# Kernel optimization log

Measured on AMD Instinct MI355X. Metric: run time of the kernel, lower is better.

Reference implementation:

```python
import jax, jax.numpy as jnp
import numpy as np

B, L, C = 256, 196, 768      # batch, tokens (14x14 grid), token_dim
K = 2048                      # codebook size (num_tokens)
H = W = 14                    # h = int(sqrt(L)), w = L // h


def setup_inputs() -> dict:
    key = jax.random.key(0)
    k1, k2, k3 = jax.random.split(key, 3)
    in_feas = jax.random.normal(k1, (B, L, C), dtype=jnp.float32)
    codebook = jax.random.normal(k2, (K, C), dtype=jnp.float32)
    # Conv1d(in=C, out=1, kernel=3, padding=1, bias=False) weight: [1, C, 3]
    att_w = jax.random.normal(k3, (1, C, 3), dtype=jnp.float32) * 0.02
    return {"in_feas": in_feas, "codebook": codebook, "att_w": att_w}


def reference(in_feas, codebook, att_w):
    b, l, c = in_feas.shape
    flat = in_feas.reshape(-1, c)  # [B*L, C]

    # --- SOHO visual-dictionary (VQ) nearest-neighbour lookup ---
    d = (jnp.sum(flat * flat, axis=1, keepdims=True)
         - 2.0 * flat @ codebook.T
         + jnp.sum(codebook * codebook, axis=1)[None, :])  # [B*L, K]
    encoding_indices = jnp.argmin(d, axis=1)               # [B*L] int
    quantized = codebook[encoding_indices]                 # [B*L, C]
    # straight-through estimator: output = x + sg(q - x)
    vd_outputs = flat + jax.lax.stop_gradient(quantized - flat)

    idx_out = encoding_indices.reshape(-1, H, W)

    # --- attention branch (att=True, not_plus=False) ---
    # Conv1d(C->1, k=3, pad=1) applied to each token as a length-1 sequence:
    # only the center tap att_w[0, :, 1] multiplies real data (neighbors are
    # zero padding), so the conv reduces to a dot with the center weights.
    att = jax.nn.relu(vd_outputs @ att_w[0, :, 1])         # [B*L]
    att_mask = jax.nn.softmax(att.reshape(b, l, 1), axis=1)  # softmax over L

    vd_outputs = vd_outputs.reshape(b, l, c)
    out_feas = vd_outputs + in_feas * att_mask
    return out_feas, idx_out
```

## Files before the change

### kernel.cpp

```cpp
#include <hip/hip_runtime.h>

#define B_ 256
#define L_ 196
#define C_ 768
#define K_ 2048
#define BL_ 50176

typedef __attribute__((ext_vector_type(8))) short bf16x8;
typedef __attribute__((ext_vector_type(4))) float f32x4;

typedef const __attribute__((address_space(1))) void gas_void;
typedef __attribute__((address_space(3))) void las_void;

__device__ __forceinline__ unsigned short f2bf(float f) {
  unsigned u = __builtin_bit_cast(unsigned, f);
  u = u + 0x7FFFu + ((u >> 16) & 1u);
  return (unsigned short)(u >> 16);
}

__device__ __forceinline__ unsigned fmono(float f) {
  unsigned u = __builtin_bit_cast(unsigned, f);
  return u ^ ((unsigned)((int)u >> 31) | 0x80000000u);
}

__global__ __launch_bounds__(256) void precompute_kernel(
    const float* __restrict__ cb, const float* __restrict__ attw,
    unsigned short* __restrict__ cbb, double* __restrict__ norms64,
    float* __restrict__ norms32, float* __restrict__ ac) {
  int wave = threadIdx.x >> 6;
  int lane = threadIdx.x & 63;
  int k = blockIdx.x * 4 + wave;
  const float* row = cb + (size_t)k * C_;
  double n = 0.0, a = 0.0;
  for (int c = lane; c < C_; c += 64) {
    float v = row[c];
    cbb[(size_t)k * C_ + c] = f2bf(v);
    n = fma((double)v, (double)v, n);
    a = fma((double)v, (double)attw[c * 3 + 1], a);
  }
  for (int off = 32; off > 0; off >>= 1) {
    n += __shfl_down(n, off);
    a += __shfl_down(a, off);
  }
  if (lane == 0) {
    norms64[k] = n;
    norms32[k] = (float)n;
    ac[k] = (a > 0.0) ? (float)a : 0.0f;
  }
}

__global__ __launch_bounds__(256) void convert_kernel(
    const float* __restrict__ x, unsigned short* __restrict__ xb) {
  int i = blockIdx.x * 256 + threadIdx.x;
  float4 v = ((const float4*)x)[i];
  uint2 w;
  w.x = (unsigned)f2bf(v.x) | ((unsigned)f2bf(v.y) << 16);
  w.y = (unsigned)f2bf(v.z) | ((unsigned)f2bf(v.w) << 16);
  ((uint2*)xb)[i] = w;
}

__global__ __launch_bounds__(512, 2) void phase1_kernel(
    const unsigned short* __restrict__ xb,
    const unsigned short* __restrict__ cbb,
    const float* __restrict__ norms32, unsigned* __restrict__ ws_cand) {
  __shared__ unsigned short lds[2][2][2][128 * 64];
  __shared__ float norms_s[256];
  __shared__ unsigned cands_s[256][12];

  int tid = threadIdx.x;
  int bid = blockIdx.x;
  int x8 = bid & 7, m = bid >> 3;
  int mblk, nblk;
  if (m < 192) {
    mblk = (m & ~7) | x8;
    nblk = m & 7;
  } else {
    mblk = m;
    nblk = x8;
  }
  size_t row0 = (size_t)mblk * 256;
  int code0 = nblk * 256;

  int wv = tid >> 6, l = tid & 63;
  int wm = wv >> 2, wn = wv & 3;
  int col16 = l & 15, quad = l >> 4;

  if (tid < 256) norms_s[tid] = norms32[code0 + tid];

  int slotraw = (tid & 7) ^ ((tid >> 3) & 7);
  const unsigned short* abase = xb + (row0 + (tid >> 3)) * (size_t)C_ +
                                (size_t)slotraw * 8;
  const unsigned short* bbase = cbb + ((size_t)code0 + (tid >> 3)) * C_ +
                                (size_t)slotraw * 8;

  auto stageA = [&](int kt, int half, int buf) {
    const unsigned short* s =
        abase + (size_t)half * 128 * C_ + (size_t)kt * 64;
    char* d = (char*)&lds[buf][0][half][0] + wv * 1024;
    __builtin_amdgcn_global_load_lds((gas_void*)s, (las_void*)d, 16, 0, 0);
    __builtin_amdgcn_global_load_lds((gas_void*)(s + (size_t)64 * C_),
                                     (las_void*)(d + 8192), 16, 0, 0);
  };
  auto stageB = [&](int kt, int half, int buf) {
    const unsigned short* s =
        bbase + (size_t)half * 128 * C_ + (size_t)kt * 64;
    char* d = (char*)&lds[buf][1][half][0] + wv * 1024;
    __builtin_amdgcn_global_load_lds((gas_void*)s, (las_void*)d, 16, 0, 0);
    __builtin_amdgcn_global_load_lds((gas_void*)(s + (size_t)64 * C_),
                                     (las_void*)(d + 8192), 16, 0, 0);
  };

  f32x4 acc[2][2][4][2];
#pragma unroll
  for (int mh = 0; mh < 2; ++mh)
#pragma unroll
    for (int nh = 0; nh < 2; ++nh)
#pragma unroll
      for (int mt = 0; mt < 4; ++mt)
#pragma unroll
        for (int nt = 0; nt < 2; ++nt)
          acc[mh][nh][mt][nt] = (f32x4){0.f, 0.f, 0.f, 0.f};

  bf16x8 af[4][2], bfr[2][2];

#define LOADA(P)                                                            \
  _Pragma("unroll") for (int mt = 0; mt < 4; ++mt)                          \
      _Pragma("unroll") for (int ks = 0; ks < 2; ++ks) af[mt][ks] =         \
      *(const bf16x8*)((P) + (wm * 64 + mt * 16 + col16) * 128 +            \
                       (((ks * 4 + quad) ^ (col16 & 7)) * 16));

#define LOADB(P)                                                            \
  _Pragma("unroll") for (int nt = 0; nt < 2; ++nt)                          \
      _Pragma("unroll") for (int ks = 0; ks < 2; ++ks) bfr[nt][ks] =        \
      *(const bf16x8*)((P) + (wn * 32 + nt * 16 + col16) * 128 +            \
                       (((ks * 4 + quad) ^ (col16 & 7)) * 16));

#define MFMA_Q(mh, nh)                                                      \
  __builtin_amdgcn_s_setprio(1);                                            \
  _Pragma("unroll") for (int mt = 0; mt < 4; ++mt)                          \
      _Pragma("unroll") for (int nt = 0; nt < 2; ++nt)                      \
          _Pragma("unroll") for (int ks = 0; ks < 2; ++ks) acc[mh][nh][mt]  \
      [nt] = __builtin_amdgcn_mfma_f32_16x16x32_bf16(                       \
          af[mt][ks], bfr[nt][ks], acc[mh][nh][mt][nt], 0, 0, 0);           \
  __builtin_amdgcn_s_setprio(0);

  stageA(0, 0, 0);
  stageB(0, 0, 0);
  stageB(0, 1, 0);
  stageA(0, 1, 0);
  asm volatile("s_waitcnt vmcnt(4)" ::: "memory");
  __builtin_amdgcn_s_barrier();

  for (int t = 0; t < 12; ++t) {
    int buf = t & 1;
    const char* A0p = (const char*)&lds[buf][0][0][0];
    const char* A1p = (const char*)&lds[buf][0][1][0];
    const char* B0p = (const char*)&lds[buf][1][0][0];
    const char* B1p = (const char*)&lds[buf][1][1][0];
    bool st = (t < 11);

    if (st) {
      stageA(t + 1, 0, buf ^ 1);
      stageB(t + 1, 0, buf ^ 1);
    }
    LOADA(A0p);
    LOADB(B0p);
    MFMA_Q(0, 0);
    if (st) {
      asm volatile("s_waitcnt vmcnt(6)" ::: "memory");
    } else {
      asm volatile("s_waitcnt vmcnt(2)" ::: "memory");
    }
    __builtin_amdgcn_s_barrier();

    if (st) stageB(t + 1, 1, buf ^ 1);
    LOADB(B1p);
    MFMA_Q(0, 1);
    if (st) {
      asm volatile("s_waitcnt vmcnt(6)" ::: "memory");
    } else {
      asm volatile("s_waitcnt vmcnt(0)" ::: "memory");
    }
    __builtin_amdgcn_s_barrier();

    if (st) stageA(t + 1, 1, buf ^ 1);
    LOADA(A1p);
    MFMA_Q(1, 1);
    LOADB(B0p);
    MFMA_Q(1, 0);
    if (st) {
      asm volatile("s_waitcnt vmcnt(4)" ::: "memory");
    }
    __builtin_amdgcn_s_barrier();
  }

#undef LOADA
#undef LOADB
#undef MFMA_Q

#pragma unroll
  for (int mh = 0; mh < 2; ++mh) {
#pragma unroll
    for (int mt = 0; mt < 4; ++mt) {
#pragma unroll
      for (int r = 0; r < 4; ++r) {
        unsigned keys[4];
#pragma unroll
        for (int nh = 0; nh < 2; ++nh)
#pragma unroll
          for (int nt = 0; nt < 2; ++nt) {
            int codel = nh * 128 + wn * 32 + nt * 16 + col16;
            float d = fmaf(-2.0f, acc[mh][nh][mt][nt][r], norms_s[codel]);
            keys[nh * 2 + nt] =
                (fmono(d) & 0xFFFFF800u) | (unsigned)(code0 + codel);
          }
        unsigned win[3];
#pragma unroll
        for (int rnd = 0; rnd < 3; ++rnd) {
          unsigned mn = min(min(keys[0], keys[1]), min(keys[2], keys[3]));
          mn = min(mn, (unsigned)__shfl_xor((int)mn, 1));
          mn = min(mn, (unsigned)__shfl_xor((int)mn, 2));
          mn = min(mn, (unsigned)__shfl_xor((int)mn, 4));
          mn = min(mn, (unsigned)__shfl_xor((int)mn, 8));
          win[rnd] = mn;
#pragma unroll
          for (int nt = 0; nt < 4; ++nt)
            if (keys[nt] == mn) keys[nt] = 0xFFFFFFFFu;
        }
        if (col16 == 0) {
          int t = mh * 128 + wm * 64 + mt * 16 + quad * 4 + r;
          cands_s[t][wn * 3 + 0] = win[0];
          cands_s[t][wn * 3 + 1] = win[1];
          cands_s[t][wn * 3 + 2] = win[2];
        }
      }
    }
  }
  __syncthreads();
  for (int i = tid; i < 256 * 12; i += 512) {
    int t = i / 12;
    int j = i - t * 12;
    ws_cand[(row0 + t) * 96 + nblk * 12 + j] = cands_s[t][j];
  }
}

__global__ __launch_bounds__(256) void phase2_kernel(
    const float* __restrict__ x, const float* __restrict__ cb,
    const unsigned* __restrict__ ws_cand, const double* __restrict__ norms64,
    int* __restrict__ out_idx) {
  __shared__ unsigned cl[32][100];
  __shared__ int rcode[32][6];
  __shared__ double rd[32][6];
  int tid = threadIdx.x;
  size_t tok0 = (size_t)blockIdx.x * 32;

  for (int i = tid; i < 32 * 96; i += 256) {
    int t = i / 96;
    int s = i - t * 96;
    cl[t][s] = ws_cand[tok0 * 96 + i];
  }
  __syncthreads();

  if (tid < 32) {
    unsigned best[6];
#pragma unroll
    for (int j = 0; j < 6; ++j) best[j] = 0xFFFFFFFFu;
    for (int s = 0; s < 96; ++s) {
      unsigned v = cl[tid][s];
      if (v < best[5]) {
        best[5] = v;
#pragma unroll
        for (int j = 5; j > 0; --j) {
          if (best[j] < best[j - 1]) {
            unsigned t = best[j];
            best[j] = best[j - 1];
            best[j - 1] = t;
          }
        }
      }
    }
#pragma unroll
    for (int j = 0; j < 6; ++j) rcode[tid][j] = (int)(best[j] & 0x7FFu);
  }
  __syncthreads();

  if (tid < 192) {
    int t = tid / 6;
    int j = tid - t * 6;
    int code = rcode[t][j];
    const float* xr = x + (tok0 + t) * (size_t)C_;
    const float* cr = cb + (size_t)code * C_;
    double s = 0.0;
    for (int c = 0; c < C_; c += 4) {
      float4 xa = *(const float4*)(xr + c);
      float4 ca = *(const float4*)(cr + c);
      s = fma((double)xa.x, (double)ca.x, s);
      s = fma((double)xa.y, (double)ca.y, s);
      s = fma((double)xa.z, (double)ca.z, s);
      s = fma((double)xa.w, (double)ca.w, s);
    }
    rd[t][j] = fma(-2.0, s, norms64[code]);
  }
  __syncthreads();

  if (tid < 32) {
    double bv = rd[tid][0];
    int bi = rcode[tid][0];
#pragma unroll
    for (int j = 1; j < 6; ++j) {
      double v = rd[tid][j];
      int i0 = rcode[tid][j];
      if (v < bv || (v == bv && i0 < bi)) {
        bv = v;
        bi = i0;
      }
    }
    out_idx[tok0 + tid] = bi;
  }
}

#define APAD 776
__global__ __launch_bounds__(256, 2) void argmin_fallback(
    const float* __restrict__ x, const float* __restrict__ cb,
    const unsigned short* __restrict__ cbb,
    const double* __restrict__ norms64, const float* __restrict__ norms32,
    int* __restrict__ out_idx) {
  __shared__ unsigned short Asf[32 * APAD];
  __shared__ float norms_s[K_];
  __shared__ unsigned int cands[32][48];
  __shared__ int rcode[32][6];
  __shared__ double rd[32][6];

  int tid = threadIdx.x;
  size_t tok0 = (size_t)blockIdx.x * 32;

  for (int i = tid; i < K_; i += 256) norms_s[i] = norms32[i];

  const float4* xin = (const float4*)(x + tok0 * C_);
  for (int i = tid; i < 32 * 192; i += 256) {
    int tok = i / 192;
    int c4 = i - tok * 192;
    float4 v = xin[i];
    uint2 w;
    w.x = (unsigned)f2bf(v.x) | ((unsigned)f2bf(v.y) << 16);
    w.y = (unsigned)f2bf(v.z) | ((unsigned)f2bf(v.w) << 16);
    *(uint2*)&Asf[tok * APAD + c4 * 4] = w;
  }
  __syncthreads();

  int wv = tid >> 6;
  int lane = tid & 63;
  int col = lane & 15;
  int quad = lane >> 4;

  const unsigned short* a0p = &Asf[(col)*APAD + quad * 8];
  const unsigned short* a1p = &Asf[(16 + col) * APAD + quad * 8];

  for (int chunk = 0; chunk < 4; ++chunk) {
    int code0 = chunk * 512 + wv * 128 + col;
    const unsigned short* bbase = cbb + (size_t)code0 * C_ + quad * 8;

    f32x4 acc[2][8];
#pragma unroll
    for (int m = 0; m < 2; ++m)
#pragma unroll
      for (int n = 0; n < 8; ++n) acc[m][n] = (f32x4){0.f, 0.f, 0.f, 0.f};

    bf16x8 ca0 = *(const bf16x8*)(a0p);
    bf16x8 ca1 = *(const bf16x8*)(a1p);
    bf16x8 cbf[8];
#pragma unroll
    for (int n = 0; n < 8; ++n)
      cbf[n] = *(const bf16x8*)(bbase + (size_t)n * 16 * C_);

    for (int ks = 0; ks < 24; ++ks) {
      bf16x8 na0, na1, nbf[8];
      if (ks < 23) {
        int k1 = (ks + 1) * 32;
        na0 = *(const bf16x8*)(a0p + k1);
        na1 = *(const bf16x8*)(a1p + k1);
#pragma unroll
        for (int n = 0; n < 8; ++n)
          nbf[n] = *(const bf16x8*)(bbase + (size_t)n * 16 * C_ + k1);
      }
#pragma unroll
      for (int n = 0; n < 8; ++n) {
        acc[0][n] = __builtin_amdgcn_mfma_f32_16x16x32_bf16(ca0, cbf[n],
                                                            acc[0][n], 0, 0, 0);
        acc[1][n] = __builtin_amdgcn_mfma_f32_16x16x32_bf16(ca1, cbf[n],
                                                            acc[1][n], 0, 0, 0);
      }
      if (ks < 23) {
        ca0 = na0;
        ca1 = na1;
#pragma unroll
        for (int n = 0; n < 8; ++n) cbf[n] = nbf[n];
      }
    }

#pragma unroll
    for (int m = 0; m < 2; ++m) {
#pragma unroll
      for (int r = 0; r < 4; ++r) {
        unsigned keys[8];
#pragma unroll
        for (int n = 0; n < 8; ++n) {
          int code = code0 + n * 16;
          float d = fmaf(-2.0f, acc[m][n][r], norms_s[code]);
          keys[n] = (fmono(d) & 0xFFFFF800u) | (unsigned)code;
        }
        unsigned win[3];
#pragma unroll
        for (int rnd = 0; rnd < 3; ++rnd) {
          unsigned mn = keys[0];
#pragma unroll
          for (int n = 1; n < 8; ++n) mn = min(mn, keys[n]);
          mn = min(mn, (unsigned)__shfl_xor((int)mn, 1));
          mn = min(mn, (unsigned)__shfl_xor((int)mn, 2));
          mn = min(mn, (unsigned)__shfl_xor((int)mn, 4));
          mn = min(mn, (unsigned)__shfl_xor((int)mn, 8));
          win[rnd] = mn;
#pragma unroll
          for (int n = 0; n < 8; ++n)
            if (keys[n] == mn) keys[n] = 0xFFFFFFFFu;
        }
        if (col == 0) {
          int token = m * 16 + quad * 4 + r;
          unsigned* cp = &cands[token][chunk * 12 + wv * 3];
          cp[0] = win[0];
          cp[1] = win[1];
          cp[2] = win[2];
        }
      }
    }
  }
  __syncthreads();

  if (tid < 32) {
    unsigned best[6];
#pragma unroll
    for (int j = 0; j < 6; ++j) best[j] = 0xFFFFFFFFu;
    for (int s = 0; s < 48; ++s) {
      unsigned v = cands[tid][s];
      if (v < best[5]) {
        best[5] = v;
#pragma unroll
        for (int j = 5; j > 0; --j) {
          if (best[j] < best[j - 1]) {
            unsigned t = best[j];
            best[j] = best[j - 1];
            best[j - 1] = t;
          }
        }
      }
    }
#pragma unroll
    for (int j = 0; j < 6; ++j) rcode[tid][j] = (int)(best[j] & 0x7FFu);
  }
  __syncthreads();

  if (tid < 192) {
    int t = tid / 6;
    int j = tid - t * 6;
    int code = rcode[t][j];
    const float* xr = x + (tok0 + t) * (size_t)C_;
    const float* cr = cb + (size_t)code * C_;
    double s = 0.0;
    for (int c = 0; c < C_; c += 4) {
      float4 xa = *(const float4*)(xr + c);
      float4 ca = *(const float4*)(cr + c);
      s = fma((double)xa.x, (double)ca.x, s);
      s = fma((double)xa.y, (double)ca.y, s);
      s = fma((double)xa.z, (double)ca.z, s);
      s = fma((double)xa.w, (double)ca.w, s);
    }
    rd[t][j] = fma(-2.0, s, norms64[code]);
  }
  __syncthreads();

  if (tid < 32) {
    double bv = rd[tid][0];
    int bi = rcode[tid][0];
#pragma unroll
    for (int j = 1; j < 6; ++j) {
      double v = rd[tid][j];
      int i0 = rcode[tid][j];
      if (v < bv || (v == bv && i0 < bi)) {
        bv = v;
        bi = i0;
      }
    }
    out_idx[tok0 + tid] = bi;
  }
}

__global__ __launch_bounds__(1024) void epilogue_kernel(
    const float* __restrict__ x, const float* __restrict__ cb,
    const float* __restrict__ ac, const int* __restrict__ idx,
    float* __restrict__ out, float* __restrict__ out_idx) {
  __shared__ float att[256];
  __shared__ float red[256];
  __shared__ int ids[L_];
  int b = blockIdx.x;
  int tid = threadIdx.x;

  float e = 0.0f;
  if (tid < 256) {
    float a = -1e30f;
    if (tid < L_) {
      int myid = idx[b * L_ + tid];
      ids[tid] = myid;
      a = ac[myid];
    }
    att[tid] = a;
    red[tid] = a;
  }
  __syncthreads();
  for (int s = 128; s > 0; s >>= 1) {
    if (tid < s) red[tid] = fmaxf(red[tid], red[tid + s]);
    __syncthreads();
  }
  float mx = red[0];
  __syncthreads();
  if (tid < 256) {
    e = (tid < L_) ? expf(att[tid] - mx) : 0.0f;
    red[tid] = e;
  }
  __syncthreads();
  for (int s = 128; s > 0; s >>= 1) {
    if (tid < s) red[tid] += red[tid + s];
    __syncthreads();
  }
  float sum = red[0];
  __syncthreads();
  if (tid < 256) att[tid] = e / sum;
  __syncthreads();

  const float4* xin = (const float4*)(x + (size_t)b * L_ * C_);
  float4* o = (float4*)(out + (size_t)b * L_ * C_);
  for (int i = tid; i < L_ * (C_ / 4); i += 1024) {
    int l = i / (C_ / 4);
    int c4 = i - l * (C_ / 4);
    const float4* crow = (const float4*)(cb + (size_t)ids[l] * C_);
    float4 xv = xin[i];
    float4 cv = crow[c4];
    float mk = att[l];
    float4 ov;
    ov.x = cv.x + xv.x * mk;
    ov.y = cv.y + xv.y * mk;
    ov.z = cv.z + xv.z * mk;
    ov.w = cv.w + xv.w * mk;
    o[i] = ov;
  }
  if (tid < L_) out_idx[b * L_ + tid] = (float)ids[tid];
}

extern "C" void kernel_launch(void* const* d_in, const int* in_sizes, int n_in,
                              void* d_out, int out_size, void* d_ws,
                              size_t ws_size, hipStream_t stream) {
  const float* in_feas = (const float*)d_in[0];
  const float* cb = (const float*)d_in[1];
  const float* attw = (const float*)d_in[2];

  char* ws = (char*)d_ws;
  size_t off = 0;
  unsigned short* cbb = (unsigned short*)(ws + off); off += 3145728;
  double* norms64 = (double*)(ws + off);           off += 16384;
  float* norms32 = (float*)(ws + off);             off += 8192;
  float* ac = (float*)(ws + off);                  off += 8192;
  int* idx = (int*)(ws + off);                     off += 200704;
  size_t base = off;
  unsigned short* xb = (unsigned short*)(ws + off); off += (size_t)BL_ * C_ * 2;
  unsigned* ws_cand = (unsigned*)(ws + off);        off += (size_t)BL_ * 96 * 4;
  size_t need_full = off;

  float* out = (float*)d_out;
  float* out_idx = out + (size_t)B_ * L_ * C_;

  precompute_kernel<<<K_ / 4, 256, 0, stream>>>(cb, attw, cbb, norms64,
                                                norms32, ac);
  if (ws_size >= need_full) {
    convert_kernel<<<BL_ * C_ / 4 / 256, 256, 0, stream>>>(in_feas, xb);
    phase1_kernel<<<dim3((BL_ / 256) * (K_ / 256)), 512, 0, stream>>>(
        xb, cbb, norms32, ws_cand);
    phase2_kernel<<<BL_ / 32, 256, 0, stream>>>(in_feas, cb, ws_cand, norms64,
                                                idx);
  } else {
    argmin_fallback<<<BL_ / 32, 256, 0, stream>>>(in_feas, cb, cbb, norms64,
                                                  norms32, idx);
  }
  epilogue_kernel<<<B_, 1024, 0, stream>>>(in_feas, cb, ac, idx, out, out_idx);
  (void)base;
}
```

Baseline: 777.9 us.

## Register-staged GEMM pipeline and split phase2 rescoring dot products across lanes

The phase1 GEMM stops using direct global-to-LDS loads with fine-grained vmcnt waits. It now loads the next K tile into registers, writes it to the other LDS buffer in the middle and at the end of the MFMA sequence, and uses a single __syncthreads per iteration. MFMA fragments are now loaded per k-slice, which uses fewer registers, and the setprio hints are dropped. Phase2 runs 768 threads and gives each candidate dot product to 4 lanes with shuffle reductions, raising parallelism in the double-precision rescoring. The trade-offs are extra register pressure for staging and more LDS write traffic in the GEMM.

```diff
diff --git a/kernel.cpp b/kernel.cpp
--- a/kernel.cpp
+++ b/kernel.cpp
@@ -93,21 +93,38 @@
   const unsigned short* bbase = cbb + ((size_t)code0 + (tid >> 3)) * C_ +
                                 (size_t)slotraw * 8;
 
-  auto stageA = [&](int kt, int half, int buf) {
-    const unsigned short* s =
-        abase + (size_t)half * 128 * C_ + (size_t)kt * 64;
-    char* d = (char*)&lds[buf][0][half][0] + wv * 1024;
-    __builtin_amdgcn_global_load_lds((gas_void*)s, (las_void*)d, 16, 0, 0);
-    __builtin_amdgcn_global_load_lds((gas_void*)(s + (size_t)64 * C_),
-                                     (las_void*)(d + 8192), 16, 0, 0);
+  uint4 aA[2][2], bB[2][2];
+  auto issueA = [&](int kt) {
+#pragma unroll
+    for (int h = 0; h < 2; ++h)
+#pragma unroll
+      for (int i = 0; i < 2; ++i)
+        aA[h][i] = *(const uint4*)(abase + (size_t)h * 128 * C_ +
+                                   (size_t)i * 64 * C_ + kt * 64);
   };
-  auto stageB = [&](int kt, int half, int buf) {
-    const unsigned short* s =
-        bbase + (size_t)half * 128 * C_ + (size_t)kt * 64;
-    char* d = (char*)&lds[buf][1][half][0] + wv * 1024;
-    __builtin_amdgcn_global_load_lds((gas_void*)s, (las_void*)d, 16, 0, 0);
-    __builtin_amdgcn_global_load_lds((gas_void*)(s + (size_t)64 * C_),
-                                     (las_void*)(d + 8192), 16, 0, 0);
+  auto issueB = [&](int kt) {
+#pragma unroll
+    for (int h = 0; h < 2; ++h)
+#pragma unroll
+      for (int i = 0; i < 2; ++i)
+        bB[h][i] = *(const uint4*)(bbase + (size_t)h * 128 * C_ +
+                                   (size_t)i * 64 * C_ + kt * 64);
+  };
+  auto writeA = [&](int wb) {
+#pragma unroll
+    for (int h = 0; h < 2; ++h)
+#pragma unroll
+      for (int i = 0; i < 2; ++i)
+        *(uint4*)((char*)&lds[wb][0][h][0] + i * 8192 + (size_t)tid * 16) =
+            aA[h][i];
+  };
+  auto writeB = [&](int wb) {
+#pragma unroll
+    for (int h = 0; h < 2; ++h)
+#pragma unroll
+      for (int i = 0; i < 2; ++i)
+        *(uint4*)((char*)&lds[wb][1][h][0] + i * 8192 + (size_t)tid * 16) =
+            bB[h][i];
   };
 
   f32x4 acc[2][2][4][2];
@@ -121,82 +138,67 @@
         for (int nt = 0; nt < 2; ++nt)
           acc[mh][nh][mt][nt] = (f32x4){0.f, 0.f, 0.f, 0.f};
 
-  bf16x8 af[4][2], bfr[2][2];
-
-#define LOADA(P)                                                            \
-  _Pragma("unroll") for (int mt = 0; mt < 4; ++mt)                          \
-      _Pragma("unroll") for (int ks = 0; ks < 2; ++ks) af[mt][ks] =         \
-      *(const bf16x8*)((P) + (wm * 64 + mt * 16 + col16) * 128 +            \
-                       (((ks * 4 + quad) ^ (col16 & 7)) * 16));
-
-#define LOADB(P)                                                            \
-  _Pragma("unroll") for (int nt = 0; nt < 2; ++nt)                          \
-      _Pragma("unroll") for (int ks = 0; ks < 2; ++ks) bfr[nt][ks] =        \
-      *(const bf16x8*)((P) + (wn * 32 + nt * 16 + col16) * 128 +            \
-                       (((ks * 4 + quad) ^ (col16 & 7)) * 16));
-
-#define MFMA_Q(mh, nh)                                                      \
-  __builtin_amdgcn_s_setprio(1);                                            \
+  bf16x8 af[4], bfr[2];
+
+#define LOADA(mh, ks)                                                       \
+  _Pragma("unroll") for (int mt = 0; mt < 4; ++mt) af[mt] =                 \
+      *(const bf16x8*)((const char*)&lds[buf][0][mh][0] +                   \
+                       (wm * 64 + mt * 16 + col16) * 128 +                  \
+                       ((((ks)*4 + quad) ^ (col16 & 7)) * 16));
+
+#define LOADB(nh, ks)                                                       \
+  _Pragma("unroll") for (int nt = 0; nt < 2; ++nt) bfr[nt] =                \
+      *(const bf16x8*)((const char*)&lds[buf][1][nh][0] +                   \
+                       (wn * 32 + nt * 16 + col16) * 128 +                  \
+                       ((((ks)*4 + quad) ^ (col16 & 7)) * 16));
+
+#define MFMA8(mh, nh)                                                       \
   _Pragma("unroll") for (int mt = 0; mt < 4; ++mt)                          \
       _Pragma("unroll") for (int nt = 0; nt < 2; ++nt)                      \
-          _Pragma("unroll") for (int ks = 0; ks < 2; ++ks) acc[mh][nh][mt]  \
-      [nt] = __builtin_amdgcn_mfma_f32_16x16x32_bf16(                       \
-          af[mt][ks], bfr[nt][ks], acc[mh][nh][mt][nt], 0, 0, 0);           \
-  __builtin_amdgcn_s_setprio(0);
-
-  stageA(0, 0, 0);
-  stageB(0, 0, 0);
-  stageB(0, 1, 0);
-  stageA(0, 1, 0);
-  asm volatile("s_waitcnt vmcnt(4)" ::: "memory");
-  __builtin_amdgcn_s_barrier();
+          acc[mh][nh][mt][nt] = __builtin_amdgcn_mfma_f32_16x16x32_bf16(    \
+              af[mt], bfr[nt], acc[mh][nh][mt][nt], 0, 0, 0);
+
+  issueA(0);
+  issueB(0);
+  writeA(0);
+  writeB(0);
+  __syncthreads();
 
   for (int t = 0; t < 12; ++t) {
     int buf = t & 1;
-    const char* A0p = (const char*)&lds[buf][0][0][0];
-    const char* A1p = (const char*)&lds[buf][0][1][0];
-    const char* B0p = (const char*)&lds[buf][1][0][0];
-    const char* B1p = (const char*)&lds[buf][1][1][0];
     bool st = (t < 11);
-
     if (st) {
-      stageA(t + 1, 0, buf ^ 1);
-      stageB(t + 1, 0, buf ^ 1);
-    }
-    LOADA(A0p);
-    LOADB(B0p);
-    MFMA_Q(0, 0);
-    if (st) {
-      asm volatile("s_waitcnt vmcnt(6)" ::: "memory");
-    } else {
-      asm volatile("s_waitcnt vmcnt(2)" ::: "memory");
-    }
-    __builtin_amdgcn_s_barrier();
-
-    if (st) stageB(t + 1, 1, buf ^ 1);
-    LOADB(B1p);
-    MFMA_Q(0, 1);
-    if (st) {
-      asm volatile("s_waitcnt vmcnt(6)" ::: "memory");
-    } else {
-      asm volatile("s_waitcnt vmcnt(0)" ::: "memory");
-    }
-    __builtin_amdgcn_s_barrier();
-
-    if (st) stageA(t + 1, 1, buf ^ 1);
-    LOADA(A1p);
-    MFMA_Q(1, 1);
-    LOADB(B0p);
-    MFMA_Q(1, 0);
-    if (st) {
-      asm volatile("s_waitcnt vmcnt(4)" ::: "memory");
-    }
-    __builtin_amdgcn_s_barrier();
+      issueA(t + 1);
+      issueB(t + 1);
+    }
+    LOADA(0, 0);
+    LOADB(0, 0);
+    MFMA8(0, 0);
+    LOADB(1, 0);
+    MFMA8(0, 1);
+    LOADA(0, 1);
+    LOADB(0, 1);
+    MFMA8(0, 0);
+    LOADB(1, 1);
+    MFMA8(0, 1);
+    if (st) writeA(buf ^ 1);
+    LOADA(1, 0);
+    LOADB(0, 0);
+    MFMA8(1, 0);
+    LOADB(1, 0);
+    MFMA8(1, 1);
+    LOADA(1, 1);
+    LOADB(0, 1);
+    MFMA8(1, 0);
+    LOADB(1, 1);
+    MFMA8(1, 1);
+    if (st) writeB(buf ^ 1);
+    __syncthreads();
   }
 
 #undef LOADA
 #undef LOADB
-#undef MFMA_Q
+#undef MFMA8
 
 #pragma unroll
   for (int mh = 0; mh < 2; ++mh) {
@@ -244,7 +246,7 @@
   }
 }
 
-__global__ __launch_bounds__(256) void phase2_kernel(
+__global__ __launch_bounds__(768) void phase2_kernel(
     const float* __restrict__ x, const float* __restrict__ cb,
     const unsigned* __restrict__ ws_cand, const double* __restrict__ norms64,
     int* __restrict__ out_idx) {
@@ -254,7 +256,7 @@
   int tid = threadIdx.x;
   size_t tok0 = (size_t)blockIdx.x * 32;
 
-  for (int i = tid; i < 32 * 96; i += 256) {
+  for (int i = tid; i < 32 * 96; i += 768) {
     int t = i / 96;
     int s = i - t * 96;
     cl[t][s] = ws_cand[tok0 * 96 + i];
@@ -284,22 +286,28 @@
   }
   __syncthreads();
 
-  if (tid < 192) {
-    int t = tid / 6;
-    int j = tid - t * 6;
-    int code = rcode[t][j];
+  {
+    int g = tid >> 2;
+    int j = tid & 3;
+    int t = g / 6;
+    int jc = g - t * 6;
+    int code = rcode[t][jc];
     const float* xr = x + (tok0 + t) * (size_t)C_;
     const float* cr = cb + (size_t)code * C_;
     double s = 0.0;
-    for (int c = 0; c < C_; c += 4) {
-      float4 xa = *(const float4*)(xr + c);
-      float4 ca = *(const float4*)(cr + c);
+#pragma unroll 4
+    for (int mm = 0; mm < 48; ++mm) {
+      int e = j * 4 + mm * 16;
+      float4 xa = *(const float4*)(xr + e);
+      float4 ca = *(const float4*)(cr + e);
       s = fma((double)xa.x, (double)ca.x, s);
       s = fma((double)xa.y, (double)ca.y, s);
       s = fma((double)xa.z, (double)ca.z, s);
       s = fma((double)xa.w, (double)ca.w, s);
     }
-    rd[t][j] = fma(-2.0, s, norms64[code]);
+    s += __shfl_xor(s, 1);
+    s += __shfl_xor(s, 2);
+    if (j == 0) rd[t][jc] = fma(-2.0, s, norms64[code]);
   }
   __syncthreads();
 
@@ -583,7 +591,7 @@
     convert_kernel<<<BL_ * C_ / 4 / 256, 256, 0, stream>>>(in_feas, xb);
     phase1_kernel<<<dim3((BL_ / 256) * (K_ / 256)), 512, 0, stream>>>(
         xb, cbb, norms32, ws_cand);
-    phase2_kernel<<<BL_ / 32, 256, 0, stream>>>(in_feas, cb, ws_cand, norms64,
+    phase2_kernel<<<BL_ / 32, 768, 0, stream>>>(in_feas, cb, ws_cand, norms64,
                                                 idx);
   } else {
     argmin_fallback<<<BL_ / 32, 256, 0, stream>>>(in_feas, cb, cbb, norms64,
```

After: 851.8 us. +9.5%, slower.
